# Kernel optimization log

Measured on AMD Instinct MI355X. Metric: run time of the kernel, lower is better.

Reference implementation:

```python
import jax, jax.numpy as jnp
import numpy as np

IN_DIM = 1024
HEAD_DIM = 64
NUM_HEADS = 16
SEQ = 4096


def setup_inputs() -> dict:
    key = jax.random.key(0)
    ks = jax.random.split(key, 7)
    s = 1.0 / np.sqrt(IN_DIM)
    return {
        "h": jax.random.normal(ks[0], (SEQ, IN_DIM), dtype=jnp.float32),
        "Wq": jax.random.uniform(ks[1], (IN_DIM, NUM_HEADS * HEAD_DIM), jnp.float32, -s, s),
        "Wk": jax.random.uniform(ks[2], (IN_DIM, NUM_HEADS * HEAD_DIM), jnp.float32, -s, s),
        "Wv": jax.random.uniform(ks[3], (IN_DIM, NUM_HEADS * HEAD_DIM), jnp.float32, -s, s),
        "bq": jax.random.uniform(ks[4], (NUM_HEADS * HEAD_DIM,), jnp.float32, -s, s),
        "bk": jax.random.uniform(ks[5], (NUM_HEADS * HEAD_DIM,), jnp.float32, -s, s),
        "bv": jax.random.uniform(ks[6], (NUM_HEADS * HEAD_DIM,), jnp.float32, -s, s),
    }


def reference(h, Wq, Wk, Wv, bq, bk, bv):
    n = h.shape[0]
    # QKV projections -> [H, S, D]
    q = (h @ Wq + bq).reshape(n, NUM_HEADS, HEAD_DIM).transpose(1, 0, 2)
    k = (h @ Wk + bk).reshape(n, NUM_HEADS, HEAD_DIM).transpose(1, 0, 2)
    v = (h @ Wv + bv).reshape(n, NUM_HEADS, HEAD_DIM).transpose(1, 0, 2)
    scale = 1.0 / np.sqrt(HEAD_DIM).astype(np.float32)
    scores = jnp.einsum('hsd,htd->hst', q, k) * scale  # [H, S, S]
    probs = jax.nn.softmax(scores, axis=-1)
    out = jnp.einsum('hst,htd->hsd', probs, v)  # [H, S, D]
    return out.transpose(1, 0, 2).reshape(n, NUM_HEADS * HEAD_DIM)
```

## Files before the change

kernel.cpp:

```cpp
#include <hip/hip_runtime.h>
#include <hip/hip_bf16.h>

#define IN_DIM    1024
#define HEAD_DIM  64
#define NUM_HEADS 16
#define SEQ       4096

#define QSCALE 0.18033688011112042f

typedef __bf16 bf16;
typedef __attribute__((ext_vector_type(4))) __bf16 bf16x4;
typedef __attribute__((ext_vector_type(8))) __bf16 bf16x8;
typedef __attribute__((ext_vector_type(4))) float floatx4;

__device__ __forceinline__ void async16(bf16* lds, const bf16* g) {
    __builtin_amdgcn_global_load_lds(
        (const __attribute__((address_space(1))) unsigned int*)g,
        (__attribute__((address_space(3))) unsigned int*)lds, 16, 0, 0);
}


__global__ void mha_conv_h(const float* __restrict__ h, bf16* __restrict__ hb) {
    int i = blockIdx.x * blockDim.x + threadIdx.x;
    float4 v = ((const float4*)h)[i];
    bf16x4 r;
    r[0] = (bf16)v.x; r[1] = (bf16)v.y; r[2] = (bf16)v.z; r[3] = (bf16)v.w;
    ((bf16x4*)hb)[i] = r;
}

__global__ void mha_conv_wt(const float* __restrict__ Wq, const float* __restrict__ Wk,
                            const float* __restrict__ Wv, bf16* __restrict__ Wt) {
    __shared__ bf16 tile[64][65];
    const int mat = blockIdx.z;
    const float* W = (mat == 0) ? Wq : (mat == 1) ? Wk : Wv;
    const int k0 = blockIdx.y * 64, n0 = blockIdx.x * 64;
    const int tn = threadIdx.x & 63, tq = threadIdx.x >> 6;
#pragma unroll
    for (int i = 0; i < 16; ++i) {
        int kk = tq + i * 4;
        tile[kk][tn] = (bf16)W[(size_t)(k0 + kk) * 1024 + n0 + tn];
    }
    __syncthreads();
#pragma unroll
    for (int i = 0; i < 16; ++i) {
        int nn = tq + i * 4;
        Wt[((size_t)mat << 20) + (size_t)(n0 + nn) * 1024 + k0 + tn] = tile[tn][nn];
    }
}

__launch_bounds__(256)
__global__ void mha_qkv_gemm(const bf16* __restrict__ hb, const bf16* __restrict__ Wt,
                             const float* __restrict__ bq, const float* __restrict__ bk,
                             const float* __restrict__ bv,
                             bf16* __restrict__ Qb, bf16* __restrict__ Kb,
                             bf16* __restrict__ Vt) {
    __shared__ __align__(16) bf16 As[128 * 32];
    __shared__ __align__(16) bf16 Bs[128 * 32];

    const int lane = threadIdx.x & 63;
    const int wave = threadIdx.x >> 6;
    const int l16  = lane & 15;
    const int quad = lane >> 4;
    const int wm   = wave & 1;
    const int wn   = wave >> 1;

    const int m0  = blockIdx.x * 128;
    const int n0  = blockIdx.y * 128;
    const int mat = n0 >> 10;
    const int nc0 = n0 & 1023;

    const bf16* Wp = Wt + ((size_t)mat << 20);

    floatx4 acc[4][4] = {};
    const int swz = (l16 >> 1) & 3;

    int g0 = wave * 128 + lane, g1 = g0 + 64;
    int row0 = g0 >> 2, gc0 = (g0 & 3) ^ ((row0 >> 1) & 3);
    int row1 = g1 >> 2, gc1 = (g1 & 3) ^ ((row1 >> 1) & 3);
    bf16* la0 = As + (size_t)(wave * 128) * 8;
    bf16* la1 = As + (size_t)(wave * 128 + 64) * 8;
    bf16* lb0 = Bs + (size_t)(wave * 128) * 8;
    bf16* lb1 = Bs + (size_t)(wave * 128 + 64) * 8;

    if (mat != 2) {
        for (int k0 = 0; k0 < IN_DIM; k0 += 32) {
            async16(la0, hb + (size_t)(m0 + row0) * IN_DIM + k0 + gc0 * 8);
            async16(la1, hb + (size_t)(m0 + row1) * IN_DIM + k0 + gc1 * 8);
            async16(lb0, Wp + (size_t)(nc0 + row0) * IN_DIM + k0 + gc0 * 8);
            async16(lb1, Wp + (size_t)(nc0 + row1) * IN_DIM + k0 + gc1 * 8);
            __syncthreads();
            bf16x8 af[4], bf[4];
#pragma unroll
            for (int mt = 0; mt < 4; ++mt)
                af[mt] = *(const bf16x8*)(As + (size_t)(wm * 64 + mt * 16 + l16) * 32
                                          + ((quad ^ swz) * 8));
#pragma unroll
            for (int nt = 0; nt < 4; ++nt)
                bf[nt] = *(const bf16x8*)(Bs + (size_t)(wn * 64 + nt * 16 + l16) * 32
                                          + ((quad ^ swz) * 8));
#pragma unroll
            for (int mt = 0; mt < 4; ++mt)
#pragma unroll
                for (int nt = 0; nt < 4; ++nt)
                    acc[mt][nt] = __builtin_amdgcn_mfma_f32_16x16x32_bf16(af[mt], bf[nt],
                                                                          acc[mt][nt], 0, 0, 0);
            __syncthreads();
        }
        const float* bias = (mat == 0) ? bq : bk;
#pragma unroll
        for (int nt = 0; nt < 4; ++nt) {
            int nc = nc0 + wn * 64 + nt * 16 + l16;
            float bb = bias[nc];
            int head = nc >> 6, d = nc & 63;
#pragma unroll
            for (int mt = 0; mt < 4; ++mt)
#pragma unroll
                for (int r = 0; r < 4; ++r) {
                    int srow = m0 + wm * 64 + mt * 16 + quad * 4 + r;
                    float v = acc[mt][nt][r] + bb;
                    if (mat == 0)
                        Qb[((size_t)head * SEQ + srow) * HEAD_DIM + d] = (bf16)(v * QSCALE);
                    else
                        Kb[((size_t)head * SEQ + srow) * HEAD_DIM + d] = (bf16)v;
                }
        }
    } else {
        for (int k0 = 0; k0 < IN_DIM; k0 += 32) {
            async16(la0, hb + (size_t)(m0 + row0) * IN_DIM + k0 + gc0 * 8);
            async16(la1, hb + (size_t)(m0 + row1) * IN_DIM + k0 + gc1 * 8);
            async16(lb0, Wp + (size_t)(nc0 + row0) * IN_DIM + k0 + gc0 * 8);
            async16(lb1, Wp + (size_t)(nc0 + row1) * IN_DIM + k0 + gc1 * 8);
            __syncthreads();
            bf16x8 af[4], bf[4];
#pragma unroll
            for (int mt = 0; mt < 4; ++mt)
                af[mt] = *(const bf16x8*)(As + (size_t)(wm * 64 + mt * 16 + l16) * 32
                                          + ((quad ^ swz) * 8));
#pragma unroll
            for (int nt = 0; nt < 4; ++nt)
                bf[nt] = *(const bf16x8*)(Bs + (size_t)(wn * 64 + nt * 16 + l16) * 32
                                          + ((quad ^ swz) * 8));
#pragma unroll
            for (int mt = 0; mt < 4; ++mt)
#pragma unroll
                for (int nt = 0; nt < 4; ++nt)
                    acc[mt][nt] = __builtin_amdgcn_mfma_f32_16x16x32_bf16(bf[nt], af[mt],
                                                                          acc[mt][nt], 0, 0, 0);
            __syncthreads();
        }
#pragma unroll
        for (int nt = 0; nt < 4; ++nt)
#pragma unroll
            for (int r = 0; r < 4; ++r) {
                int n = nc0 + wn * 64 + nt * 16 + quad * 4 + r;
                float bb = bv[n];
                int head = n >> 6, d = n & 63;
#pragma unroll
                for (int mt = 0; mt < 4; ++mt) {
                    int s = m0 + wm * 64 + mt * 16 + l16;
                    Vt[((size_t)head * 64 + d) * SEQ + s] = (bf16)(acc[mt][nt][r] + bb);
                }
            }
    }
}

template<int TS>
__launch_bounds__(256, 2)
__global__ void mha_attn(const bf16* __restrict__ Qb, const bf16* __restrict__ Kb,
                         const bf16* __restrict__ Vt, float* __restrict__ Op,
                         float* __restrict__ Lp, float* __restrict__ out) {
    __shared__ __align__(16) bf16 Ks[2][64 * 64];
    __shared__ __align__(16) bf16 Vs[2][64 * 64];
    __shared__ __align__(16) bf16 Ps[16][16 * 72];

    const int lane = threadIdx.x & 63;
    const int wave = threadIdx.x >> 6;
    const int l16  = lane & 15;
    const int quad = lane >> 4;

    const int hh    = blockIdx.y;
    const int zz    = blockIdx.z;
    const int qbase = blockIdx.x * 256 + wave * 64;
    const int tbase = zz * (64 / TS);
    const int niter = 64 / TS;

    const bf16* Qh = Qb + (size_t)hh * SEQ * HEAD_DIM;
    const bf16* Kh = Kb + (size_t)hh * SEQ * HEAD_DIM;
    const bf16* Vh = Vt + (size_t)hh * HEAD_DIM * SEQ;

    const int g0 = wave * 128 + lane, g1 = g0 + 64;
    const int sr0 = g0 >> 3, sc0 = (g0 & 7) ^ (sr0 & 7);
    const int sr1 = g1 >> 3, sc1 = (g1 & 7) ^ (sr1 & 7);

    bf16x8 qf[4][2];
#pragma unroll
    for (int m = 0; m < 4; ++m)
#pragma unroll
        for (int ks = 0; ks < 2; ++ks)
            qf[m][ks] = *(const bf16x8*)(Qh + (size_t)(qbase + m * 16 + l16) * HEAD_DIM
                                         + ks * 32 + quad * 8);

    bf16x8 vone;
#pragma unroll
    for (int i = 0; i < 8; ++i) vone[i] = (bf16)1.0f;

    floatx4 o[4][4] = {};
    floatx4 ol[4]   = {};

    const int swk = l16 & 7;

    auto stage = [&](int slot, int t) {
        async16(&Ks[slot][(wave * 128) * 8],      Kh + (size_t)(t * 64 + sr0) * HEAD_DIM + sc0 * 8);
        async16(&Ks[slot][(wave * 128 + 64) * 8], Kh + (size_t)(t * 64 + sr1) * HEAD_DIM + sc1 * 8);
        async16(&Vs[slot][(wave * 128) * 8],      Vh + (size_t)sr0 * SEQ + t * 64 + sc0 * 8);
        async16(&Vs[slot][(wave * 128 + 64) * 8], Vh + (size_t)sr1 * SEQ + t * 64 + sc1 * 8);
    };

    stage(0, tbase);
    __syncthreads();

    for (int t = 0; t < niter; ++t) {
        const int cur = t & 1;
        if (t < niter - 1) stage(cur ^ 1, tbase + t + 1);

        bf16x8 kf[4][2];
#pragma unroll
        for (int tt = 0; tt < 4; ++tt)
#pragma unroll
            for (int ks = 0; ks < 2; ++ks)
                kf[tt][ks] = *(const bf16x8*)(&Ks[cur][(size_t)(tt * 16 + l16) * 64
                                              + (((ks * 4 + quad) ^ swk) * 8)]);
#pragma unroll
        for (int m = 0; m < 4; ++m) {
            bf16* lp = &Ps[wave * 4 + m][0];
#pragma unroll
            for (int tt = 0; tt < 4; ++tt) {
                floatx4 s = {};
                s = __builtin_amdgcn_mfma_f32_16x16x32_bf16(kf[tt][0], qf[m][0], s, 0, 0, 0);
                s = __builtin_amdgcn_mfma_f32_16x16x32_bf16(kf[tt][1], qf[m][1], s, 0, 0, 0);
                bf16x4 pk;
#pragma unroll
                for (int r = 0; r < 4; ++r) pk[r] = (bf16)__builtin_amdgcn_exp2f(s[r]);
                *(bf16x4*)(lp + l16 * 72 + tt * 16 + quad * 4) = pk;
            }
        }

        bf16x8 vf[4][2];
#pragma unroll
        for (int dt = 0; dt < 4; ++dt)
#pragma unroll
            for (int ks = 0; ks < 2; ++ks)
                vf[dt][ks] = *(const bf16x8*)(&Vs[cur][(size_t)(dt * 16 + l16) * 64
                                              + (((ks * 4 + quad) ^ swk) * 8)]);
#pragma unroll
        for (int m = 0; m < 4; ++m) {
            bf16* lp = &Ps[wave * 4 + m][0];
#pragma unroll
            for (int ks = 0; ks < 2; ++ks) {
                bf16x8 pf = *(const bf16x8*)(lp + l16 * 72 + ks * 32 + quad * 8);
#pragma unroll
                for (int dt = 0; dt < 4; ++dt)
                    o[m][dt] = __builtin_amdgcn_mfma_f32_16x16x32_bf16(pf, vf[dt][ks],
                                                                       o[m][dt], 0, 0, 0);
                ol[m] = __builtin_amdgcn_mfma_f32_16x16x32_bf16(pf, vone, ol[m], 0, 0, 0);
            }
        }
        __syncthreads();
    }

    if (TS == 1) {
#pragma unroll
        for (int m = 0; m < 4; ++m)
#pragma unroll
            for (int r = 0; r < 4; ++r) {
                float inv = 1.0f / ol[m][r];
                int srow = qbase + m * 16 + quad * 4 + r;
#pragma unroll
                for (int dt = 0; dt < 4; ++dt)
                    out[(size_t)srow * (NUM_HEADS * HEAD_DIM) + hh * 64 + dt * 16 + l16]
                        = o[m][dt][r] * inv;
            }
    } else {
        float* Oz = Op + ((size_t)(zz * NUM_HEADS + hh) * SEQ) * HEAD_DIM;
        float* Lz = Lp + (size_t)(zz * NUM_HEADS + hh) * SEQ;
#pragma unroll
        for (int m = 0; m < 4; ++m)
#pragma unroll
            for (int r = 0; r < 4; ++r) {
                int srow = qbase + m * 16 + quad * 4 + r;
#pragma unroll
                for (int dt = 0; dt < 4; ++dt)
                    Oz[(size_t)srow * HEAD_DIM + dt * 16 + l16] = o[m][dt][r];
                if (l16 == 0) Lz[srow] = ol[m][r];
            }
    }
}

__global__ void mha_combine(const float* __restrict__ Op, const float* __restrict__ Lp,
                            float* __restrict__ out) {
    int i = blockIdx.x * blockDim.x + threadIdx.x;
    int j = i * 4;
    int s = j >> 10, rem = j & 1023, hh = rem >> 6, d = rem & 63;
    size_t i0 = ((size_t)hh * SEQ + s) * HEAD_DIM + d;
    size_t i1 = ((size_t)(NUM_HEADS + hh) * SEQ + s) * HEAD_DIM + d;
    float4 a = *(const float4*)(Op + i0);
    float4 b = *(const float4*)(Op + i1);
    float l = Lp[(size_t)hh * SEQ + s] + Lp[(size_t)(NUM_HEADS + hh) * SEQ + s];
    float inv = 1.0f / l;
    float4 r;
    r.x = (a.x + b.x) * inv; r.y = (a.y + b.y) * inv;
    r.z = (a.z + b.z) * inv; r.w = (a.w + b.w) * inv;
    *(float4*)(out + j) = r;
}

extern "C" void kernel_launch(void* const* d_in, const int* in_sizes, int n_in,
                              void* d_out, int out_size, void* d_ws, size_t ws_size,
                              hipStream_t stream) {
    const float* h  = (const float*)d_in[0];
    const float* Wq = (const float*)d_in[1];
    const float* Wk = (const float*)d_in[2];
    const float* Wv = (const float*)d_in[3];
    const float* bq = (const float*)d_in[4];
    const float* bk = (const float*)d_in[5];
    const float* bv = (const float*)d_in[6];
    float* out = (float*)d_out;

    char* ws = (char*)d_ws;
    const size_t MB = 1024 * 1024;
    bf16* Qb = (bf16*)(ws);
    bf16* Kb = (bf16*)(ws + 8 * MB);
    bf16* Vt = (bf16*)(ws + 16 * MB);
    bf16* hb = (bf16*)(ws + 24 * MB);
    bf16* Wt = (bf16*)(ws + 32 * MB);
    float* Op = (float*)(ws + 24 * MB);
    float* Lp = (float*)(ws + 24 * MB + (size_t)2 * NUM_HEADS * SEQ * HEAD_DIM * 4);

    const size_t NEED = 24 * MB + (size_t)2 * NUM_HEADS * SEQ * HEAD_DIM * 4
                      + (size_t)2 * NUM_HEADS * SEQ * 4;
    const bool split = (ws_size >= NEED);

    mha_conv_h<<<(SEQ * IN_DIM / 4) / 256, 256, 0, stream>>>(h, hb);
    mha_conv_wt<<<dim3(16, 16, 3), 256, 0, stream>>>(Wq, Wk, Wv, Wt);
    mha_qkv_gemm<<<dim3(SEQ / 128, (3 * IN_DIM) / 128), 256, 0, stream>>>(
        hb, Wt, bq, bk, bv, Qb, Kb, Vt);
    if (split) {
        mha_attn<2><<<dim3(SEQ / 256, NUM_HEADS, 2), 256, 0, stream>>>(
            Qb, Kb, Vt, Op, Lp, out);
        mha_combine<<<(SEQ * IN_DIM / 4) / 256, 256, 0, stream>>>(Op, Lp, out);
    } else {
        mha_attn<1><<<dim3(SEQ / 256, NUM_HEADS, 1), 256, 0, stream>>>(
            Qb, Kb, Vt, Op, Lp, out);
    }
}
```

Baseline: 212.5 us.

## Software-pipeline attention: overlap QK^T/exp of next tile with PV of previous

Splits the attention loop into an S stage (QK^T plus exp2, written to per-wave LDS) and a PV stage, then skews them so iteration t computes S for tile t while running the PV MFMAs for tile t-1. V gets a third LDS buffer so the V tile for t-1 stays resident while tiles t and t+1 are in flight. The P and V fragments for the lagged tile are loaded into registers before the S stage. The aim is to interleave exp and conversion work with matrix ops and hide LDS latency. The cost is more VGPR pressure under the 2-blocks-per-CU launch bound, plus 8KB more LDS, which may reduce occupancy or cause spills.

```diff
diff --git a/kernel.cpp b/kernel.cpp
--- a/kernel.cpp
+++ b/kernel.cpp
@@ -170,7 +170,7 @@
                          const bf16* __restrict__ Vt, float* __restrict__ Op,
                          float* __restrict__ Lp, float* __restrict__ out) {
     __shared__ __align__(16) bf16 Ks[2][64 * 64];
-    __shared__ __align__(16) bf16 Vs[2][64 * 64];
+    __shared__ __align__(16) bf16 Vs[3][64 * 64];
     __shared__ __align__(16) bf16 Ps[16][16 * 72];
 
     const int lane = threadIdx.x & 63;
@@ -181,8 +181,8 @@
     const int hh    = blockIdx.y;
     const int zz    = blockIdx.z;
     const int qbase = blockIdx.x * 256 + wave * 64;
-    const int tbase = zz * (64 / TS);
     const int niter = 64 / TS;
+    const int tbase = zz * niter;
 
     const bf16* Qh = Qb + (size_t)hh * SEQ * HEAD_DIM;
     const bf16* Kh = Kb + (size_t)hh * SEQ * HEAD_DIM;
@@ -209,26 +209,22 @@
 
     const int swk = l16 & 7;
 
-    auto stage = [&](int slot, int t) {
+    auto stageK = [&](int slot, int t) {
         async16(&Ks[slot][(wave * 128) * 8],      Kh + (size_t)(t * 64 + sr0) * HEAD_DIM + sc0 * 8);
         async16(&Ks[slot][(wave * 128 + 64) * 8], Kh + (size_t)(t * 64 + sr1) * HEAD_DIM + sc1 * 8);
+    };
+    auto stageV = [&](int slot, int t) {
         async16(&Vs[slot][(wave * 128) * 8],      Vh + (size_t)sr0 * SEQ + t * 64 + sc0 * 8);
         async16(&Vs[slot][(wave * 128 + 64) * 8], Vh + (size_t)sr1 * SEQ + t * 64 + sc1 * 8);
     };
 
-    stage(0, tbase);
-    __syncthreads();
-
-    for (int t = 0; t < niter; ++t) {
-        const int cur = t & 1;
-        if (t < niter - 1) stage(cur ^ 1, tbase + t + 1);
-
+    auto doS = [&](int kslot) {
         bf16x8 kf[4][2];
 #pragma unroll
         for (int tt = 0; tt < 4; ++tt)
 #pragma unroll
             for (int ks = 0; ks < 2; ++ks)
-                kf[tt][ks] = *(const bf16x8*)(&Ks[cur][(size_t)(tt * 16 + l16) * 64
+                kf[tt][ks] = *(const bf16x8*)(&Ks[kslot][(size_t)(tt * 16 + l16) * 64
                                               + (((ks * 4 + quad) ^ swk) * 8)]);
 #pragma unroll
         for (int m = 0; m < 4; ++m) {
@@ -244,29 +240,50 @@
                 *(bf16x4*)(lp + l16 * 72 + tt * 16 + quad * 4) = pk;
             }
         }
-
-        bf16x8 vf[4][2];
+    };
+
+    bf16x8 pf[4][2], vfr[4][2];
+    auto loadPV = [&](int vslot) {
+#pragma unroll
+        for (int m = 0; m < 4; ++m)
+#pragma unroll
+            for (int ks = 0; ks < 2; ++ks)
+                pf[m][ks] = *(const bf16x8*)(&Ps[wave * 4 + m][0] + l16 * 72 + ks * 32 + quad * 8);
 #pragma unroll
         for (int dt = 0; dt < 4; ++dt)
 #pragma unroll
             for (int ks = 0; ks < 2; ++ks)
-                vf[dt][ks] = *(const bf16x8*)(&Vs[cur][(size_t)(dt * 16 + l16) * 64
-                                              + (((ks * 4 + quad) ^ swk) * 8)]);
-#pragma unroll
-        for (int m = 0; m < 4; ++m) {
-            bf16* lp = &Ps[wave * 4 + m][0];
+                vfr[dt][ks] = *(const bf16x8*)(&Vs[vslot][(size_t)(dt * 16 + l16) * 64
+                                               + (((ks * 4 + quad) ^ swk) * 8)]);
+    };
+    auto doPV = [&]() {
+#pragma unroll
+        for (int m = 0; m < 4; ++m)
 #pragma unroll
             for (int ks = 0; ks < 2; ++ks) {
-                bf16x8 pf = *(const bf16x8*)(lp + l16 * 72 + ks * 32 + quad * 8);
 #pragma unroll
                 for (int dt = 0; dt < 4; ++dt)
-                    o[m][dt] = __builtin_amdgcn_mfma_f32_16x16x32_bf16(pf, vf[dt][ks],
+                    o[m][dt] = __builtin_amdgcn_mfma_f32_16x16x32_bf16(pf[m][ks], vfr[dt][ks],
                                                                        o[m][dt], 0, 0, 0);
-                ol[m] = __builtin_amdgcn_mfma_f32_16x16x32_bf16(pf, vone, ol[m], 0, 0, 0);
-            }
-        }
+                ol[m] = __builtin_amdgcn_mfma_f32_16x16x32_bf16(pf[m][ks], vone, ol[m], 0, 0, 0);
+            }
+    };
+
+    stageK(0, tbase); stageV(0, tbase);
+    __syncthreads();
+    if (niter > 1) { stageK(1, tbase + 1); stageV(1 % 3, tbase + 1); }
+    doS(0);
+    __syncthreads();
+
+    for (int t = 1; t < niter; ++t) {
+        if (t + 1 < niter) { stageK((t + 1) & 1, tbase + t + 1); stageV((t + 1) % 3, tbase + t + 1); }
+        loadPV((t - 1) % 3);
+        doS(t & 1);
+        doPV();
         __syncthreads();
     }
+    loadPV((niter - 1) % 3);
+    doPV();
 
     if (TS == 1) {
 #pragma unroll
```

Measured after the change: 214.4 us. About the same (+0.9%).

## Keep attention probabilities in registers via transposed MFMA and add 4-way KV split

Applied to the files above, without the earlier changes.

The attention kernel stops writing exp'd scores to LDS and reading them back. It keeps P in registers as bf16x4 fragments and computes O transposed with 16x16x16 bf16 MFMAs against V fragments loaded directly from swizzled LDS. Row sums are now gathered with VALU adds and cross-lane shuffles instead of an extra MFMA against a ones vector. Occupancy is raised to 3 blocks per SIMD in launch bounds, and when the workspace is large enough the key range is split four ways, with a templated combine kernel summing the partial results. This trades a larger partial-sum buffer and more combine traffic for more parallelism and less LDS traffic.

```diff
diff --git a/kernel.cpp b/kernel.cpp
--- a/kernel.cpp
+++ b/kernel.cpp
@@ -12,11 +12,25 @@
 typedef __attribute__((ext_vector_type(4))) __bf16 bf16x4;
 typedef __attribute__((ext_vector_type(8))) __bf16 bf16x8;
 typedef __attribute__((ext_vector_type(4))) float floatx4;
+typedef __attribute__((ext_vector_type(4))) short s16x4;
 
 __device__ __forceinline__ void async16(bf16* lds, const bf16* g) {
     __builtin_amdgcn_global_load_lds(
         (const __attribute__((address_space(1))) unsigned int*)g,
         (__attribute__((address_space(3))) unsigned int*)lds, 16, 0, 0);
+}
+
+__device__ __forceinline__ floatx4 mfma16(bf16x4 a, bf16x4 b, floatx4 c) {
+#if __has_builtin(__builtin_amdgcn_mfma_f32_16x16x16bf16_1k)
+    union U { bf16x4 h; s16x4 s; };
+    U ua, ub; ua.h = a; ub.h = b;
+    return __builtin_amdgcn_mfma_f32_16x16x16bf16_1k(ua.s, ub.s, c, 0, 0, 0);
+#else
+    bf16 z = (bf16)0.f;
+    bf16x8 a8 = {a[0], a[1], a[2], a[3], z, z, z, z};
+    bf16x8 b8 = {b[0], b[1], b[2], b[3], z, z, z, z};
+    return __builtin_amdgcn_mfma_f32_16x16x32_bf16(a8, b8, c, 0, 0, 0);
+#endif
 }
 
 
@@ -165,13 +179,12 @@
 }
 
 template<int TS>
-__launch_bounds__(256, 2)
+__launch_bounds__(256, 3)
 __global__ void mha_attn(const bf16* __restrict__ Qb, const bf16* __restrict__ Kb,
                          const bf16* __restrict__ Vt, float* __restrict__ Op,
                          float* __restrict__ Lp, float* __restrict__ out) {
     __shared__ __align__(16) bf16 Ks[2][64 * 64];
     __shared__ __align__(16) bf16 Vs[2][64 * 64];
-    __shared__ __align__(16) bf16 Ps[16][16 * 72];
 
     const int lane = threadIdx.x & 63;
     const int wave = threadIdx.x >> 6;
@@ -181,8 +194,8 @@
     const int hh    = blockIdx.y;
     const int zz    = blockIdx.z;
     const int qbase = blockIdx.x * 256 + wave * 64;
-    const int tbase = zz * (64 / TS);
     const int niter = 64 / TS;
+    const int tbase = zz * niter;
 
     const bf16* Qh = Qb + (size_t)hh * SEQ * HEAD_DIM;
     const bf16* Kh = Kb + (size_t)hh * SEQ * HEAD_DIM;
@@ -200,12 +213,8 @@
             qf[m][ks] = *(const bf16x8*)(Qh + (size_t)(qbase + m * 16 + l16) * HEAD_DIM
                                          + ks * 32 + quad * 8);
 
-    bf16x8 vone;
-#pragma unroll
-    for (int i = 0; i < 8; ++i) vone[i] = (bf16)1.0f;
-
     floatx4 o[4][4] = {};
-    floatx4 ol[4]   = {};
+    float ls[4] = {0.f, 0.f, 0.f, 0.f};
 
     const int swk = l16 & 7;
 
@@ -221,7 +230,7 @@
 
     for (int t = 0; t < niter; ++t) {
         const int cur = t & 1;
-        if (t < niter - 1) stage(cur ^ 1, tbase + t + 1);
+        if (t + 1 < niter) stage(cur ^ 1, tbase + t + 1);
 
         bf16x8 kf[4][2];
 #pragma unroll
@@ -230,86 +239,104 @@
             for (int ks = 0; ks < 2; ++ks)
                 kf[tt][ks] = *(const bf16x8*)(&Ks[cur][(size_t)(tt * 16 + l16) * 64
                                               + (((ks * 4 + quad) ^ swk) * 8)]);
+
+        bf16x4 vaf[4][4];
+#pragma unroll
+        for (int dt = 0; dt < 4; ++dt)
+#pragma unroll
+            for (int c = 0; c < 4; ++c) {
+                int row = dt * 16 + l16;
+                int boff = row * 128 + (((c * 2 + (quad >> 1)) ^ (row & 7)) * 16)
+                         + (quad & 1) * 8;
+                vaf[dt][c] = *(const bf16x4*)((const char*)&Vs[cur][0] + boff);
+            }
+
 #pragma unroll
         for (int m = 0; m < 4; ++m) {
-            bf16* lp = &Ps[wave * 4 + m][0];
+            bf16x4 pfr[4];
 #pragma unroll
             for (int tt = 0; tt < 4; ++tt) {
                 floatx4 s = {};
                 s = __builtin_amdgcn_mfma_f32_16x16x32_bf16(kf[tt][0], qf[m][0], s, 0, 0, 0);
                 s = __builtin_amdgcn_mfma_f32_16x16x32_bf16(kf[tt][1], qf[m][1], s, 0, 0, 0);
                 bf16x4 pk;
-#pragma unroll
-                for (int r = 0; r < 4; ++r) pk[r] = (bf16)__builtin_amdgcn_exp2f(s[r]);
-                *(bf16x4*)(lp + l16 * 72 + tt * 16 + quad * 4) = pk;
-            }
-        }
-
-        bf16x8 vf[4][2];
-#pragma unroll
-        for (int dt = 0; dt < 4; ++dt)
-#pragma unroll
-            for (int ks = 0; ks < 2; ++ks)
-                vf[dt][ks] = *(const bf16x8*)(&Vs[cur][(size_t)(dt * 16 + l16) * 64
-                                              + (((ks * 4 + quad) ^ swk) * 8)]);
+                float sum = 0.f;
+#pragma unroll
+                for (int r = 0; r < 4; ++r) {
+                    float e = __builtin_amdgcn_exp2f(s[r]);
+                    sum += e;
+                    pk[r] = (bf16)e;
+                }
+                ls[m] += sum;
+                pfr[tt] = pk;
+            }
+#pragma unroll
+            for (int dt = 0; dt < 4; ++dt)
+#pragma unroll
+                for (int c = 0; c < 4; ++c)
+                    o[m][dt] = mfma16(vaf[dt][c], pfr[c], o[m][dt]);
+        }
+        __syncthreads();
+    }
+
+#pragma unroll
+    for (int m = 0; m < 4; ++m) {
+        ls[m] += __shfl_xor(ls[m], 16, 64);
+        ls[m] += __shfl_xor(ls[m], 32, 64);
+    }
+
+    if (TS == 1) {
 #pragma unroll
         for (int m = 0; m < 4; ++m) {
-            bf16* lp = &Ps[wave * 4 + m][0];
-#pragma unroll
-            for (int ks = 0; ks < 2; ++ks) {
-                bf16x8 pf = *(const bf16x8*)(lp + l16 * 72 + ks * 32 + quad * 8);
-#pragma unroll
-                for (int dt = 0; dt < 4; ++dt)
-                    o[m][dt] = __builtin_amdgcn_mfma_f32_16x16x32_bf16(pf, vf[dt][ks],
-                                                                       o[m][dt], 0, 0, 0);
-                ol[m] = __builtin_amdgcn_mfma_f32_16x16x32_bf16(pf, vone, ol[m], 0, 0, 0);
-            }
-        }
-        __syncthreads();
-    }
-
-    if (TS == 1) {
-#pragma unroll
-        for (int m = 0; m < 4; ++m)
-#pragma unroll
-            for (int r = 0; r < 4; ++r) {
-                float inv = 1.0f / ol[m][r];
-                int srow = qbase + m * 16 + quad * 4 + r;
-#pragma unroll
-                for (int dt = 0; dt < 4; ++dt)
-                    out[(size_t)srow * (NUM_HEADS * HEAD_DIM) + hh * 64 + dt * 16 + l16]
-                        = o[m][dt][r] * inv;
-            }
+            float inv = 1.0f / ls[m];
+            int srow = qbase + m * 16 + l16;
+#pragma unroll
+            for (int dt = 0; dt < 4; ++dt) {
+                float4 r;
+                r.x = o[m][dt][0] * inv; r.y = o[m][dt][1] * inv;
+                r.z = o[m][dt][2] * inv; r.w = o[m][dt][3] * inv;
+                *(float4*)(out + (size_t)srow * (NUM_HEADS * HEAD_DIM)
+                           + hh * 64 + dt * 16 + quad * 4) = r;
+            }
+        }
     } else {
         float* Oz = Op + ((size_t)(zz * NUM_HEADS + hh) * SEQ) * HEAD_DIM;
         float* Lz = Lp + (size_t)(zz * NUM_HEADS + hh) * SEQ;
 #pragma unroll
-        for (int m = 0; m < 4; ++m)
-#pragma unroll
-            for (int r = 0; r < 4; ++r) {
-                int srow = qbase + m * 16 + quad * 4 + r;
-#pragma unroll
-                for (int dt = 0; dt < 4; ++dt)
-                    Oz[(size_t)srow * HEAD_DIM + dt * 16 + l16] = o[m][dt][r];
-                if (l16 == 0) Lz[srow] = ol[m][r];
-            }
-    }
-}
-
+        for (int m = 0; m < 4; ++m) {
+            int srow = qbase + m * 16 + l16;
+#pragma unroll
+            for (int dt = 0; dt < 4; ++dt) {
+                float4 r;
+                r.x = o[m][dt][0]; r.y = o[m][dt][1];
+                r.z = o[m][dt][2]; r.w = o[m][dt][3];
+                *(float4*)(Oz + (size_t)srow * HEAD_DIM + dt * 16 + quad * 4) = r;
+            }
+            if (quad == 0) Lz[srow] = ls[m];
+        }
+    }
+}
+
+template<int NS>
 __global__ void mha_combine(const float* __restrict__ Op, const float* __restrict__ Lp,
                             float* __restrict__ out) {
     int i = blockIdx.x * blockDim.x + threadIdx.x;
     int j = i * 4;
     int s = j >> 10, rem = j & 1023, hh = rem >> 6, d = rem & 63;
-    size_t i0 = ((size_t)hh * SEQ + s) * HEAD_DIM + d;
-    size_t i1 = ((size_t)(NUM_HEADS + hh) * SEQ + s) * HEAD_DIM + d;
-    float4 a = *(const float4*)(Op + i0);
-    float4 b = *(const float4*)(Op + i1);
-    float l = Lp[(size_t)hh * SEQ + s] + Lp[(size_t)(NUM_HEADS + hh) * SEQ + s];
+    const size_t OS = (size_t)NUM_HEADS * SEQ * HEAD_DIM;
+    const size_t LS = (size_t)NUM_HEADS * SEQ;
+    size_t base = ((size_t)hh * SEQ + s) * HEAD_DIM + d;
+    float4 acc = {0.f, 0.f, 0.f, 0.f};
+    float l = 0.f;
+#pragma unroll
+    for (int z = 0; z < NS; ++z) {
+        float4 a = *(const float4*)(Op + z * OS + base);
+        acc.x += a.x; acc.y += a.y; acc.z += a.z; acc.w += a.w;
+        l += Lp[z * LS + (size_t)hh * SEQ + s];
+    }
     float inv = 1.0f / l;
     float4 r;
-    r.x = (a.x + b.x) * inv; r.y = (a.y + b.y) * inv;
-    r.z = (a.z + b.z) * inv; r.w = (a.w + b.w) * inv;
+    r.x = acc.x * inv; r.y = acc.y * inv; r.z = acc.z * inv; r.w = acc.w * inv;
     *(float4*)(out + j) = r;
 }
 
@@ -332,23 +359,28 @@
     bf16* Vt = (bf16*)(ws + 16 * MB);
     bf16* hb = (bf16*)(ws + 24 * MB);
     bf16* Wt = (bf16*)(ws + 32 * MB);
+
+    const size_t OSZ = (size_t)NUM_HEADS * SEQ * HEAD_DIM * 4;
+    const size_t LSZ = (size_t)NUM_HEADS * SEQ * 4;
     float* Op = (float*)(ws + 24 * MB);
-    float* Lp = (float*)(ws + 24 * MB + (size_t)2 * NUM_HEADS * SEQ * HEAD_DIM * 4);
-
-    const size_t NEED = 24 * MB + (size_t)2 * NUM_HEADS * SEQ * HEAD_DIM * 4
-                      + (size_t)2 * NUM_HEADS * SEQ * 4;
-    const bool split = (ws_size >= NEED);
 
     mha_conv_h<<<(SEQ * IN_DIM / 4) / 256, 256, 0, stream>>>(h, hb);
     mha_conv_wt<<<dim3(16, 16, 3), 256, 0, stream>>>(Wq, Wk, Wv, Wt);
     mha_qkv_gemm<<<dim3(SEQ / 128, (3 * IN_DIM) / 128), 256, 0, stream>>>(
         hb, Wt, bq, bk, bv, Qb, Kb, Vt);
-    if (split) {
+
+    if (ws_size >= 24 * MB + 4 * (OSZ + LSZ)) {
+        float* Lp = (float*)(ws + 24 * MB + 4 * OSZ);
+        mha_attn<4><<<dim3(SEQ / 256, NUM_HEADS, 4), 256, 0, stream>>>(
+            Qb, Kb, Vt, Op, Lp, out);
+        mha_combine<4><<<(SEQ * IN_DIM / 4) / 256, 256, 0, stream>>>(Op, Lp, out);
+    } else if (ws_size >= 24 * MB + 2 * (OSZ + LSZ)) {
+        float* Lp = (float*)(ws + 24 * MB + 2 * OSZ);
         mha_attn<2><<<dim3(SEQ / 256, NUM_HEADS, 2), 256, 0, stream>>>(
             Qb, Kb, Vt, Op, Lp, out);
-        mha_combine<<<(SEQ * IN_DIM / 4) / 256, 256, 0, stream>>>(Op, Lp, out);
+        mha_combine<2><<<(SEQ * IN_DIM / 4) / 256, 256, 0, stream>>>(Op, Lp, out);
     } else {
         mha_attn<1><<<dim3(SEQ / 256, NUM_HEADS, 1), 256, 0, stream>>>(
-            Qb, Kb, Vt, Op, Lp, out);
-    }
-}
+            Qb, Kb, Vt, nullptr, nullptr, out);
+    }
+}
```

New measurement: 430.7 us. +102.6%, slower.
